# Optimization experiments

Measured on AMD Instinct MI355X. Metric: run time of the kernel, lower is better.

## Reference

```python
import jax, jax.numpy as jnp
import numpy as np
from jax import lax

T, D, H = 8192, 1024, 1024
FORGET_BIAS = 1.0  # BasicLSTMCell default


def setup_inputs() -> dict:
    key = jax.random.key(0)
    ks = jax.random.split(key, 5)
    x = jax.random.normal(ks[0], (T, D), dtype=jnp.float32)
    c_in = jax.random.normal(ks[1], (1, H), dtype=jnp.float32)
    h_in = jax.random.normal(ks[2], (1, H), dtype=jnp.float32)
    # BasicLSTMCell kernel [D+H, 4H], gates ordered (i, j, f, o); glorot-ish scale
    W_lstm = jax.random.normal(ks[3], (D + H, 4 * H), dtype=jnp.float32) * (1.0 / np.sqrt(D + H))
    b_lstm = jnp.zeros((4 * H,), dtype=jnp.float32)
    # normc_initializer(1.0): columns normalized to unit norm
    W_out = jax.random.normal(ks[4], (H, H), dtype=jnp.float32)
    W_out = W_out / jnp.linalg.norm(W_out, axis=0, keepdims=True)
    b_out = jnp.zeros((H,), dtype=jnp.float32)
    return {"x": x, "c_in": c_in, "h_in": h_in, "W_lstm": W_lstm,
            "b_lstm": b_lstm, "W_out": W_out, "b_out": b_out}


def reference(x, c_in, h_in, W_lstm, b_lstm, W_out, b_out):
    # Precompute the input contribution for all timesteps in one big GEMM;
    # the recurrence only needs the h @ W_h part per step.
    Wx, Wh = W_lstm[:D], W_lstm[D:]          # [D,4H], [H,4H]
    xz = x @ Wx + b_lstm                      # [T, 4H]

    def step(carry, xz_t):
        c, h = carry                          # [H], [H]
        z = xz_t + h @ Wh                     # [4H]
        i, j, f, o = jnp.split(z, 4)
        new_c = c * jax.nn.sigmoid(f + FORGET_BIAS) + jax.nn.sigmoid(i) * jnp.tanh(j)
        new_h = jnp.tanh(new_c) * jax.nn.sigmoid(o)
        return (new_c, new_h), new_h

    (c_last, h_last), hs = lax.scan(step, (c_in[0], h_in[0]), xz)  # hs: [T, H]
    output = hs @ W_out + b_out               # final_layer (no activation)
    return output, c_last[None, :], h_last[None, :]
```

## Files before the change

### kernel.cpp

```cpp
#include <hip/hip_runtime.h>

#define T_STEPS 8192
#define DD 1024
#define HH 1024
#define NWG 256
#define NTHR 512
#define SCOPE_AGENT __HIP_MEMORY_SCOPE_AGENT
typedef unsigned long long u64;

__device__ __forceinline__ int swz(int k) { return k ^ ((((k) >> 6) & 3) << 2); }

__device__ __forceinline__ float fsig(float v) {
  return 1.f / (1.f + __expf(-v));
}
__device__ __forceinline__ float ftanh(float v) {
  return 2.f / (1.f + __expf(-2.f * v)) - 1.f;
}

__global__ __launch_bounds__(NTHR, 1) void lstm_scan(
    const float* __restrict__ x, const float* __restrict__ c_in,
    const float* __restrict__ h_in, const float* __restrict__ W,
    const float* __restrict__ b, float* __restrict__ Hs,
    u64* __restrict__ hbuf,
    float* __restrict__ out_tail)
{
  const int g = blockIdx.x, tid = threadIdx.x;
  const int lane = tid & 63, wave = tid >> 6;
  const int col = tid & 15, seg = tid >> 4;
  const int gate = col >> 2, hi = col & 3;
  const int cg = gate * HH + g * 4 + hi;

  __shared__ float Wl[32768];
  __shared__ float xb[DD];
  __shared__ float hb[HH];
  __shared__ float partial[8][16];

  float c_reg = 0.f, hlast = 0.f;

  if (tid < 4) {
    const float h0 = h_in[g * 4 + tid];
    c_reg = c_in[g * 4 + tid];
    const u64 pv = ((u64)1u << 32) | (u64)__float_as_uint(h0);
    __hip_atomic_store(&hbuf[g * 4 + tid], pv, __ATOMIC_RELAXED, SCOPE_AGENT);
  }

  #pragma unroll
  for (int j = 0; j < 16; ++j) {
    float4 v;
    v.x = W[(size_t)(seg * 64 + j * 4 + 0) * (4 * HH) + cg];
    v.y = W[(size_t)(seg * 64 + j * 4 + 1) * (4 * HH) + cg];
    v.z = W[(size_t)(seg * 64 + j * 4 + 2) * (4 * HH) + cg];
    v.w = W[(size_t)(seg * 64 + j * 4 + 3) * (4 * HH) + cg];
    *(float4*)&Wl[(wave * 16 + j) * 256 + lane * 4] = v;
  }

  const float bias_reg = b[((lane & 15) >> 2) * HH + g * 4 + (lane & 3)];

  float xv0 = x[tid], xv1 = x[tid + 512];

  __syncthreads();

  const bool is_x = (wave < 4);

  for (int t = 1; t <= T_STEPS; ++t) {
    xb[swz(tid)]       = xv0;
    xb[swz(tid + 512)] = xv1;
    __syncthreads();

    if (t < T_STEPS) {
      const float* xn = x + (size_t)t * DD;
      xv0 = xn[tid];
      xv1 = xn[tid + 512];
    }

    if (is_x) {
      float p = 0.f;
      #pragma unroll
      for (int j = 0; j < 16; ++j) {
        const float4 wv = *(const float4*)&Wl[(wave * 16 + j) * 256 + lane * 4];
        const float4 xv = *(const float4*)&xb[(seg * 64 + j * 4) ^ ((seg & 3) << 2)];
        p = fmaf(xv.x, wv.x, p); p = fmaf(xv.y, wv.y, p);
        p = fmaf(xv.z, wv.z, p); p = fmaf(xv.w, wv.w, p);
      }
      p += __shfl_xor(p, 16);
      p += __shfl_xor(p, 32);
      if (lane < 16) partial[wave][lane] = p;
    } else {
      const u64* hp = hbuf + ((t - 1) & 1) * HH;
      const int cb = (wave - 4) * 256;
      const unsigned tg = (unsigned)t;
      u64 a0 = __hip_atomic_load(&hp[cb + lane],       __ATOMIC_RELAXED, SCOPE_AGENT);
      u64 a1 = __hip_atomic_load(&hp[cb + 64 + lane],  __ATOMIC_RELAXED, SCOPE_AGENT);
      u64 a2 = __hip_atomic_load(&hp[cb + 128 + lane], __ATOMIC_RELAXED, SCOPE_AGENT);
      u64 a3 = __hip_atomic_load(&hp[cb + 192 + lane], __ATOMIC_RELAXED, SCOPE_AGENT);
      bool r0 = (unsigned)(a0 >> 32) >= tg;
      bool r1 = (unsigned)(a1 >> 32) >= tg;
      bool r2 = (unsigned)(a2 >> 32) >= tg;
      bool r3 = (unsigned)(a3 >> 32) >= tg;
      while (!(r0 & r1 & r2 & r3)) {
        if (!r0) { a0 = __hip_atomic_load(&hp[cb + lane],       __ATOMIC_RELAXED, SCOPE_AGENT); r0 = (unsigned)(a0 >> 32) >= tg; }
        if (!r1) { a1 = __hip_atomic_load(&hp[cb + 64 + lane],  __ATOMIC_RELAXED, SCOPE_AGENT); r1 = (unsigned)(a1 >> 32) >= tg; }
        if (!r2) { a2 = __hip_atomic_load(&hp[cb + 128 + lane], __ATOMIC_RELAXED, SCOPE_AGENT); r2 = (unsigned)(a2 >> 32) >= tg; }
        if (!r3) { a3 = __hip_atomic_load(&hp[cb + 192 + lane], __ATOMIC_RELAXED, SCOPE_AGENT); r3 = (unsigned)(a3 >> 32) >= tg; }
      }
      hb[swz(cb + lane)]       = __uint_as_float((unsigned)a0);
      hb[swz(cb + 64 + lane)]  = __uint_as_float((unsigned)a1);
      hb[swz(cb + 128 + lane)] = __uint_as_float((unsigned)a2);
      hb[swz(cb + 192 + lane)] = __uint_as_float((unsigned)a3);
      asm volatile("s_waitcnt lgkmcnt(0)" ::: "memory");
      const int s2 = seg - 16;
      float q = 0.f;
      #pragma unroll
      for (int j = 0; j < 16; ++j) {
        const float4 wv = *(const float4*)&Wl[(wave * 16 + j) * 256 + lane * 4];
        const float4 hv = *(const float4*)&hb[(s2 * 64 + j * 4) ^ ((s2 & 3) << 2)];
        q = fmaf(hv.x, wv.x, q); q = fmaf(hv.y, wv.y, q);
        q = fmaf(hv.z, wv.z, q); q = fmaf(hv.w, wv.w, q);
      }
      q += __shfl_xor(q, 16);
      q += __shfl_xor(q, 32);
      if (lane < 16) partial[wave][lane] = q;
    }
    __syncthreads();

    if (wave == 0) {
      float zsum = bias_reg;
      #pragma unroll
      for (int wv = 0; wv < 8; ++wv) zsum += partial[wv][lane & 15];
      const int gt = (lane & 15) >> 2;
      const float zin = (gt == 1) ? (2.f * zsum) : (gt == 2 ? zsum + 1.f : zsum);
      const float s = 1.f / (1.f + __expf(-zin));
      const float act = (gt == 1) ? (2.f * s - 1.f) : s;
      const float ig = __shfl(act, tid);
      const float tj = __shfl(act, tid + 4);
      const float fg = __shfl(act, tid + 8);
      const float og = __shfl(act, tid + 12);
      if (tid < 4) {
        const float nc = c_reg * fg + ig * tj;
        const float nh = ftanh(nc) * og;
        c_reg = nc; hlast = nh;
        const u64 pv = ((u64)(unsigned)(t + 1) << 32) | (u64)__float_as_uint(nh);
        __hip_atomic_store(&hbuf[(t & 1) * HH + g * 4 + tid], pv,
                           __ATOMIC_RELAXED, SCOPE_AGENT);
        Hs[(size_t)(t - 1) * HH + g * 4 + tid] = nh;
      }
    }
  }

  if (tid < 4) {
    out_tail[g * 4 + tid]      = c_reg;
    out_tail[HH + g * 4 + tid] = hlast;
  }
}

#define BM 128
#define BN 128
#define BK 16
__device__ __forceinline__ int bswz(int c) { return c ^ (((c >> 5) & 1) << 2); }

__global__ __launch_bounds__(256, 2) void out_gemm(
    const float* __restrict__ A,
    const float* __restrict__ Bw,
    const float* __restrict__ bias,
    float* __restrict__ C)
{
  __shared__ float As[BK][BM + 4];
  __shared__ float Bs[BK][BN + 4];
  const int tid = threadIdx.x;
  const int row0 = blockIdx.y * BM, col0 = blockIdx.x * BN;
  const int tx = tid & 15, ty = tid >> 4;

  const int ar = tid >> 1;
  const int ac = (tid & 1) * 8;
  const int br = tid >> 4;
  const int bc = (tid & 15) * 8;

  float acc[8][8];
  #pragma unroll
  for (int i = 0; i < 8; ++i)
    #pragma unroll
    for (int j = 0; j < 8; ++j) acc[i][j] = 0.f;

  for (int k0 = 0; k0 < HH; k0 += BK) {
    const float4 a0 = *(const float4*)&A[(size_t)(row0 + ar) * HH + k0 + ac];
    const float4 a1 = *(const float4*)&A[(size_t)(row0 + ar) * HH + k0 + ac + 4];
    const float4 b0 = *(const float4*)&Bw[(size_t)(k0 + br) * HH + col0 + bc];
    const float4 b1 = *(const float4*)&Bw[(size_t)(k0 + br) * HH + col0 + bc + 4];
    As[ac + 0][ar] = a0.x; As[ac + 1][ar] = a0.y;
    As[ac + 2][ar] = a0.z; As[ac + 3][ar] = a0.w;
    As[ac + 4][ar] = a1.x; As[ac + 5][ar] = a1.y;
    As[ac + 6][ar] = a1.z; As[ac + 7][ar] = a1.w;
    *(float4*)&Bs[br][bswz(bc)]     = b0;
    *(float4*)&Bs[br][bswz(bc + 4)] = b1;
    __syncthreads();
    #pragma unroll
    for (int kk = 0; kk < BK; ++kk) {
      float a[8], bb[8];
      *(float4*)&a[0]  = *(const float4*)&As[kk][ty * 8];
      *(float4*)&a[4]  = *(const float4*)&As[kk][ty * 8 + 4];
      *(float4*)&bb[0] = *(const float4*)&Bs[kk][bswz(tx * 8)];
      *(float4*)&bb[4] = *(const float4*)&Bs[kk][bswz(tx * 8 + 4)];
      #pragma unroll
      for (int i = 0; i < 8; ++i)
        #pragma unroll
        for (int j = 0; j < 8; ++j)
          acc[i][j] = fmaf(a[i], bb[j], acc[i][j]);
    }
    __syncthreads();
  }

  #pragma unroll
  for (int i = 0; i < 8; ++i) {
    const size_t r = (size_t)(row0 + ty * 8 + i) * HH;
    #pragma unroll
    for (int j = 0; j < 8; j += 4) {
      float4 v;
      v.x = acc[i][j + 0] + bias[col0 + tx * 8 + j + 0];
      v.y = acc[i][j + 1] + bias[col0 + tx * 8 + j + 1];
      v.z = acc[i][j + 2] + bias[col0 + tx * 8 + j + 2];
      v.w = acc[i][j + 3] + bias[col0 + tx * 8 + j + 3];
      *(float4*)&C[r + col0 + tx * 8 + j] = v;
    }
  }
}

extern "C" void kernel_launch(void* const* d_in, const int* in_sizes, int n_in,
                              void* d_out, int out_size, void* d_ws, size_t ws_size,
                              hipStream_t stream) {
  const float* x    = (const float*)d_in[0];
  const float* c_in = (const float*)d_in[1];
  const float* h_in = (const float*)d_in[2];
  const float* W    = (const float*)d_in[3];
  const float* b    = (const float*)d_in[4];
  const float* Wout = (const float*)d_in[5];
  const float* bout = (const float*)d_in[6];
  float* out = (float*)d_out;

  u64* hbuf = (u64*)d_ws;
  float* Hs = (float*)(hbuf + 2 * HH);
  float* out_tail = out + (size_t)T_STEPS * HH;

  hipMemsetAsync(hbuf, 0, 2 * HH * sizeof(u64), stream);

  void* args[] = {(void*)&x, (void*)&c_in, (void*)&h_in, (void*)&W, (void*)&b,
                  (void*)&Hs, (void*)&hbuf, (void*)&out_tail};
  hipLaunchCooperativeKernel((void*)lstm_scan, dim3(NWG), dim3(NTHR),
                             args, 0, stream);

  out_gemm<<<dim3(HH / BN, T_STEPS / BM), 256, 0, stream>>>(Hs, Wout, bout, out);
}
```

Measured before the change: 12.99 ms.

## Split x/h waves with LDS flag handoff and per-wave gate epilogue

Restructures the per-step loop so x-projection waves and h-recurrence waves run separate loops. The h waves signal readiness through shared-memory flags and each computes its own output unit's gate activations, instead of one wave handling the epilogue after a barrier. The aim is to take one of the two block barriers, and the serial wave-0 epilogue, off the critical path of the recurrence. It also splits the dot-product accumulation into four chains for more ILP, vectorises the x prefetch, and adds s_sleep in the spin loop. In exchange it relies on relaxed LDS flag ordering and mismatched __syncthreads call sites in divergent branches, which risks races.

```diff
diff --git a/kernel.cpp b/kernel.cpp
--- a/kernel.cpp
+++ b/kernel.cpp
@@ -6,13 +6,11 @@
 #define NWG 256
 #define NTHR 512
 #define SCOPE_AGENT __HIP_MEMORY_SCOPE_AGENT
+#define SCOPE_WG __HIP_MEMORY_SCOPE_WORKGROUP
 typedef unsigned long long u64;
 
 __device__ __forceinline__ int swz(int k) { return k ^ ((((k) >> 6) & 3) << 2); }
 
-__device__ __forceinline__ float fsig(float v) {
-  return 1.f / (1.f + __expf(-v));
-}
 __device__ __forceinline__ float ftanh(float v) {
   return 2.f / (1.f + __expf(-2.f * v)) - 1.f;
 }
@@ -34,12 +32,11 @@
   __shared__ float xb[DD];
   __shared__ float hb[HH];
   __shared__ float partial[8][16];
-
-  float c_reg = 0.f, hlast = 0.f;
-
+  __shared__ int pflag[8];
+
+  if (tid < 8) pflag[tid] = 0;
   if (tid < 4) {
     const float h0 = h_in[g * 4 + tid];
-    c_reg = c_in[g * 4 + tid];
     const u64 pv = ((u64)1u << 32) | (u64)__float_as_uint(h0);
     __hip_atomic_store(&hbuf[g * 4 + tid], pv, __ATOMIC_RELAXED, SCOPE_AGENT);
   }
@@ -54,40 +51,71 @@
     *(float4*)&Wl[(wave * 16 + j) * 256 + lane * 4] = v;
   }
 
-  const float bias_reg = b[((lane & 15) >> 2) * HH + g * 4 + (lane & 3)];
-
-  float xv0 = x[tid], xv1 = x[tid + 512];
-
-  __syncthreads();
-
   const bool is_x = (wave < 4);
 
-  for (int t = 1; t <= T_STEPS; ++t) {
-    xb[swz(tid)]       = xv0;
-    xb[swz(tid + 512)] = xv1;
+  if (is_x) {
+    const int sw = (seg & 3) << 2;
+    float4 xq = *(const float4*)&x[wave * 256 + lane * 4];
     __syncthreads();
 
-    if (t < T_STEPS) {
-      const float* xn = x + (size_t)t * DD;
-      xv0 = xn[tid];
-      xv1 = xn[tid + 512];
-    }
-
-    if (is_x) {
-      float p = 0.f;
+    for (int t = 1; t <= T_STEPS; ++t) {
+      *(float4*)&xb[swz(wave * 256 + lane * 4)] = xq;
+      if (t < T_STEPS)
+        xq = *(const float4*)&x[(size_t)t * DD + wave * 256 + lane * 4];
+      asm volatile("s_waitcnt lgkmcnt(0)" ::: "memory");
+      float q0 = 0.f, q1 = 0.f, q2 = 0.f, q3 = 0.f;
       #pragma unroll
-      for (int j = 0; j < 16; ++j) {
-        const float4 wv = *(const float4*)&Wl[(wave * 16 + j) * 256 + lane * 4];
-        const float4 xv = *(const float4*)&xb[(seg * 64 + j * 4) ^ ((seg & 3) << 2)];
-        p = fmaf(xv.x, wv.x, p); p = fmaf(xv.y, wv.y, p);
-        p = fmaf(xv.z, wv.z, p); p = fmaf(xv.w, wv.w, p);
-      }
+      for (int j4 = 0; j4 < 4; ++j4) {
+        {
+          const int j = j4 * 4 + 0;
+          const float4 wv = *(const float4*)&Wl[(wave * 16 + j) * 256 + lane * 4];
+          const float4 xv = *(const float4*)&xb[(seg * 64 + j * 4) ^ sw];
+          q0 = fmaf(xv.x, wv.x, q0); q0 = fmaf(xv.y, wv.y, q0);
+          q0 = fmaf(xv.z, wv.z, q0); q0 = fmaf(xv.w, wv.w, q0);
+        }
+        {
+          const int j = j4 * 4 + 1;
+          const float4 wv = *(const float4*)&Wl[(wave * 16 + j) * 256 + lane * 4];
+          const float4 xv = *(const float4*)&xb[(seg * 64 + j * 4) ^ sw];
+          q1 = fmaf(xv.x, wv.x, q1); q1 = fmaf(xv.y, wv.y, q1);
+          q1 = fmaf(xv.z, wv.z, q1); q1 = fmaf(xv.w, wv.w, q1);
+        }
+        {
+          const int j = j4 * 4 + 2;
+          const float4 wv = *(const float4*)&Wl[(wave * 16 + j) * 256 + lane * 4];
+          const float4 xv = *(const float4*)&xb[(seg * 64 + j * 4) ^ sw];
+          q2 = fmaf(xv.x, wv.x, q2); q2 = fmaf(xv.y, wv.y, q2);
+          q2 = fmaf(xv.z, wv.z, q2); q2 = fmaf(xv.w, wv.w, q2);
+        }
+        {
+          const int j = j4 * 4 + 3;
+          const float4 wv = *(const float4*)&Wl[(wave * 16 + j) * 256 + lane * 4];
+          const float4 xv = *(const float4*)&xb[(seg * 64 + j * 4) ^ sw];
+          q3 = fmaf(xv.x, wv.x, q3); q3 = fmaf(xv.y, wv.y, q3);
+          q3 = fmaf(xv.z, wv.z, q3); q3 = fmaf(xv.w, wv.w, q3);
+        }
+      }
+      float p = (q0 + q1) + (q2 + q3);
       p += __shfl_xor(p, 16);
       p += __shfl_xor(p, 32);
       if (lane < 16) partial[wave][lane] = p;
-    } else {
+      asm volatile("s_waitcnt lgkmcnt(0)" ::: "memory");
+      if (lane == 0)
+        __hip_atomic_store(&pflag[wave], t, __ATOMIC_RELAXED, SCOPE_WG);
+      __syncthreads();
+    }
+  } else {
+    const int e = wave - 4;
+    const int cb = e * 256;
+    const int s2 = seg - 16;
+    const int sw2 = (s2 & 3) << 2;
+    const float biasF = (lane < 4) ? b[lane * HH + g * 4 + e] : 0.f;
+    float c_reg = (lane == 0) ? c_in[g * 4 + e] : 0.f;
+    float hlast = 0.f;
+    __syncthreads();
+
+    for (int t = 1; t <= T_STEPS; ++t) {
       const u64* hp = hbuf + ((t - 1) & 1) * HH;
-      const int cb = (wave - 4) * 256;
       const unsigned tg = (unsigned)t;
       u64 a0 = __hip_atomic_load(&hp[cb + lane],       __ATOMIC_RELAXED, SCOPE_AGENT);
       u64 a1 = __hip_atomic_load(&hp[cb + 64 + lane],  __ATOMIC_RELAXED, SCOPE_AGENT);
@@ -98,6 +126,7 @@
       bool r2 = (unsigned)(a2 >> 32) >= tg;
       bool r3 = (unsigned)(a3 >> 32) >= tg;
       while (!(r0 & r1 & r2 & r3)) {
+        __builtin_amdgcn_s_sleep(1);
         if (!r0) { a0 = __hip_atomic_load(&hp[cb + lane],       __ATOMIC_RELAXED, SCOPE_AGENT); r0 = (unsigned)(a0 >> 32) >= tg; }
         if (!r1) { a1 = __hip_atomic_load(&hp[cb + 64 + lane],  __ATOMIC_RELAXED, SCOPE_AGENT); r1 = (unsigned)(a1 >> 32) >= tg; }
         if (!r2) { a2 = __hip_atomic_load(&hp[cb + 128 + lane], __ATOMIC_RELAXED, SCOPE_AGENT); r2 = (unsigned)(a2 >> 32) >= tg; }
@@ -108,48 +137,88 @@
       hb[swz(cb + 128 + lane)] = __uint_as_float((unsigned)a2);
       hb[swz(cb + 192 + lane)] = __uint_as_float((unsigned)a3);
       asm volatile("s_waitcnt lgkmcnt(0)" ::: "memory");
-      const int s2 = seg - 16;
-      float q = 0.f;
+      float q0 = 0.f, q1 = 0.f, q2 = 0.f, q3 = 0.f;
       #pragma unroll
-      for (int j = 0; j < 16; ++j) {
-        const float4 wv = *(const float4*)&Wl[(wave * 16 + j) * 256 + lane * 4];
-        const float4 hv = *(const float4*)&hb[(s2 * 64 + j * 4) ^ ((s2 & 3) << 2)];
-        q = fmaf(hv.x, wv.x, q); q = fmaf(hv.y, wv.y, q);
-        q = fmaf(hv.z, wv.z, q); q = fmaf(hv.w, wv.w, q);
-      }
+      for (int j4 = 0; j4 < 4; ++j4) {
+        {
+          const int j = j4 * 4 + 0;
+          const float4 wv = *(const float4*)&Wl[(wave * 16 + j) * 256 + lane * 4];
+          const float4 hv = *(const float4*)&hb[(s2 * 64 + j * 4) ^ sw2];
+          q0 = fmaf(hv.x, wv.x, q0); q0 = fmaf(hv.y, wv.y, q0);
+          q0 = fmaf(hv.z, wv.z, q0); q0 = fmaf(hv.w, wv.w, q0);
+        }
+        {
+          const int j = j4 * 4 + 1;
+          const float4 wv = *(const float4*)&Wl[(wave * 16 + j) * 256 + lane * 4];
+          const float4 hv = *(const float4*)&hb[(s2 * 64 + j * 4) ^ sw2];
+          q1 = fmaf(hv.x, wv.x, q1); q1 = fmaf(hv.y, wv.y, q1);
+          q1 = fmaf(hv.z, wv.z, q1); q1 = fmaf(hv.w, wv.w, q1);
+        }
+        {
+          const int j = j4 * 4 + 2;
+          const float4 wv = *(const float4*)&Wl[(wave * 16 + j) * 256 + lane * 4];
+          const float4 hv = *(const float4*)&hb[(s2 * 64 + j * 4) ^ sw2];
+          q2 = fmaf(hv.x, wv.x, q2); q2 = fmaf(hv.y, wv.y, q2);
+          q2 = fmaf(hv.z, wv.z, q2); q2 = fmaf(hv.w, wv.w, q2);
+        }
+        {
+          const int j = j4 * 4 + 3;
+          const float4 wv = *(const float4*)&Wl[(wave * 16 + j) * 256 + lane * 4];
+          const float4 hv = *(const float4*)&hb[(s2 * 64 + j * 4) ^ sw2];
+          q3 = fmaf(hv.x, wv.x, q3); q3 = fmaf(hv.y, wv.y, q3);
+          q3 = fmaf(hv.z, wv.z, q3); q3 = fmaf(hv.w, wv.w, q3);
+        }
+      }
+      float q = (q0 + q1) + (q2 + q3);
       q += __shfl_xor(q, 16);
       q += __shfl_xor(q, 32);
       if (lane < 16) partial[wave][lane] = q;
-    }
-    __syncthreads();
-
-    if (wave == 0) {
-      float zsum = bias_reg;
-      #pragma unroll
-      for (int wv = 0; wv < 8; ++wv) zsum += partial[wv][lane & 15];
-      const int gt = (lane & 15) >> 2;
-      const float zin = (gt == 1) ? (2.f * zsum) : (gt == 2 ? zsum + 1.f : zsum);
-      const float s = 1.f / (1.f + __expf(-zin));
-      const float act = (gt == 1) ? (2.f * s - 1.f) : s;
-      const float ig = __shfl(act, tid);
-      const float tj = __shfl(act, tid + 4);
-      const float fg = __shfl(act, tid + 8);
-      const float og = __shfl(act, tid + 12);
-      if (tid < 4) {
+      asm volatile("s_waitcnt lgkmcnt(0)" ::: "memory");
+      if (lane == 0)
+        __hip_atomic_store(&pflag[wave], t, __ATOMIC_RELAXED, SCOPE_WG);
+      for (;;) {
+        const int f0 = __hip_atomic_load(&pflag[0], __ATOMIC_RELAXED, SCOPE_WG);
+        const int f1 = __hip_atomic_load(&pflag[1], __ATOMIC_RELAXED, SCOPE_WG);
+        const int f2 = __hip_atomic_load(&pflag[2], __ATOMIC_RELAXED, SCOPE_WG);
+        const int f3 = __hip_atomic_load(&pflag[3], __ATOMIC_RELAXED, SCOPE_WG);
+        const int f4 = __hip_atomic_load(&pflag[4], __ATOMIC_RELAXED, SCOPE_WG);
+        const int f5 = __hip_atomic_load(&pflag[5], __ATOMIC_RELAXED, SCOPE_WG);
+        const int f6 = __hip_atomic_load(&pflag[6], __ATOMIC_RELAXED, SCOPE_WG);
+        const int f7 = __hip_atomic_load(&pflag[7], __ATOMIC_RELAXED, SCOPE_WG);
+        if (f0 >= t && f1 >= t && f2 >= t && f3 >= t &&
+            f4 >= t && f5 >= t && f6 >= t && f7 >= t) break;
+      }
+      float act = 0.f;
+      if (lane < 4) {
+        const int ci = lane * 4 + e;
+        const float s01 = partial[0][ci] + partial[1][ci];
+        const float s23 = partial[2][ci] + partial[3][ci];
+        const float s45 = partial[4][ci] + partial[5][ci];
+        const float s67 = partial[6][ci] + partial[7][ci];
+        const float z = biasF + ((s01 + s23) + (s45 + s67));
+        const float zin = (lane == 1) ? (2.f * z) : (lane == 2 ? z + 1.f : z);
+        const float s = 1.f / (1.f + __expf(-zin));
+        act = (lane == 1) ? (2.f * s - 1.f) : s;
+      }
+      const float ig = __shfl(act, 0);
+      const float tj = __shfl(act, 1);
+      const float fg = __shfl(act, 2);
+      const float og = __shfl(act, 3);
+      if (lane == 0) {
         const float nc = c_reg * fg + ig * tj;
         const float nh = ftanh(nc) * og;
         c_reg = nc; hlast = nh;
         const u64 pv = ((u64)(unsigned)(t + 1) << 32) | (u64)__float_as_uint(nh);
-        __hip_atomic_store(&hbuf[(t & 1) * HH + g * 4 + tid], pv,
+        __hip_atomic_store(&hbuf[(t & 1) * HH + g * 4 + e], pv,
                            __ATOMIC_RELAXED, SCOPE_AGENT);
-        Hs[(size_t)(t - 1) * HH + g * 4 + tid] = nh;
-      }
-    }
-  }
-
-  if (tid < 4) {
-    out_tail[g * 4 + tid]      = c_reg;
-    out_tail[HH + g * 4 + tid] = hlast;
+        Hs[(size_t)(t - 1) * HH + g * 4 + e] = nh;
+      }
+      __syncthreads();
+    }
+    if (lane == 0) {
+      out_tail[g * 4 + e]      = c_reg;
+      out_tail[HH + g * 4 + e] = hlast;
+    }
   }
 }
 
```

New measurement: 32.50 ms. 150% more time.
